# Optimization experiments

Hardware: AMD Instinct MI355X
Metric: run time of the kernel (lower is better)

## Reference

```python
import jax, jax.numpy as jnp
from jax import lax
import numpy as np

IN_DIM, HID, B, T = 64, 512, 256, 512


def _lstm_layer(xs, W_ih, W_hh, b_ih, b_hh):
    # xs: [B, T, D_in]; W_ih: [4H, D_in]; W_hh: [4H, H]; biases: [4H]
    Bn = xs.shape[0]
    H = W_hh.shape[1]
    # Precompute input projection for all timesteps (one big GEMM).
    x_proj = jnp.einsum('btd,gd->btg', xs, W_ih) + b_ih + b_hh  # [B, T, 4H]

    def step(carry, xp):
        h, c = carry
        g = xp + h @ W_hh.T  # [B, 4H], PyTorch gate order: i, f, g, o
        i, f, gg, o = jnp.split(g, 4, axis=-1)
        i = jax.nn.sigmoid(i)
        f = jax.nn.sigmoid(f)
        gg = jnp.tanh(gg)
        o = jax.nn.sigmoid(o)
        c = f * c + i * gg
        h = o * jnp.tanh(c)
        return (h, c), h

    z = jnp.zeros((Bn, H), xs.dtype)
    _, hs = lax.scan(step, (z, z), jnp.swapaxes(x_proj, 0, 1))  # [T, B, H]
    return jnp.swapaxes(hs, 0, 1)  # [B, T, H]


def setup_inputs() -> dict:
    key = jax.random.key(0)
    ks = jax.random.split(key, 16)
    s_in = 1.0 / np.sqrt(HID)
    u = lambda k, shp: jax.random.uniform(k, shp, jnp.float32, -s_in, s_in)
    return {
        'x': jax.random.normal(ks[0], (B, T, IN_DIM), jnp.float32),
        'W_ih0': u(ks[1], (4 * HID, IN_DIM)),
        'W_hh0': u(ks[2], (4 * HID, HID)),
        'b_ih0': u(ks[3], (4 * HID,)),
        'b_hh0': u(ks[4], (4 * HID,)),
        'W_ih1': u(ks[5], (4 * HID, HID)),
        'W_hh1': u(ks[6], (4 * HID, HID)),
        'b_ih1': u(ks[7], (4 * HID,)),
        'b_hh1': u(ks[8], (4 * HID,)),
        'W1': u(ks[9], (HID // 2, HID)),
        'b1': u(ks[10], (HID // 2,)),
        'W2': u(ks[11], (1, HID // 2)),
        'b2': u(ks[12], (1,)),
    }


def reference(x, W_ih0, W_hh0, b_ih0, b_hh0, W_ih1, W_hh1, b_ih1, b_hh1, W1, b1, W2, b2):
    h1 = _lstm_layer(x, W_ih0, W_hh0, b_ih0, b_hh0)   # [B, T, H]
    h2 = _lstm_layer(h1, W_ih1, W_hh1, b_ih1, b_hh1)  # [B, T, H] (inference: no inter-layer dropout)
    last = h2[:, -1, :]                                # final timestep
    hidden = jax.nn.relu(last @ W1.T + b1)
    return jax.nn.sigmoid(hidden @ W2.T + b2)          # [B, 1]
```

## Files before the change

### kernel.cpp

```cpp
#include <hip/hip_runtime.h>
#include <hip/hip_bf16.h>
#include <stdint.h>


#define Bsz 256
#define Tsz 512
#define IND 64
#define Hsz 512
#define BH (Bsz * Hsz)
#define P1S 66

typedef __attribute__((ext_vector_type(8))) short short8;
typedef __attribute__((ext_vector_type(4))) float floatx4;

static __device__ __forceinline__ short f2bf(float f) {
    unsigned u = __float_as_uint(f);
    u += 0x7FFFu + ((u >> 16) & 1u);
    return (short)(u >> 16);
}
static __device__ __forceinline__ float bf2f(short s) {
    return __uint_as_float(((unsigned)(unsigned short)s) << 16);
}
static __device__ __forceinline__ float sigm(float z) { return 1.f / (1.f + __expf(-z)); }
static __device__ __forceinline__ float tanh_f(float z) { return 2.f / (1.f + __expf(-2.f * z)) - 1.f; }

static __device__ __forceinline__ short8 ring16(const short* p) {
    short8 v;
    asm volatile("global_load_dwordx4 %0, %1, off sc1" : "=v"(v) : "v"(p));
    return v;
}

__global__ __launch_bounds__(512, 1) void lstm_pers(
    const float* __restrict__ x,
    const float* __restrict__ Wih0, const float* __restrict__ Whh0,
    const float* __restrict__ bih0, const float* __restrict__ bhh0,
    const float* __restrict__ Wih1, const float* __restrict__ Whh1,
    const float* __restrict__ bih1, const float* __restrict__ bhh1,
    int* __restrict__ slots, short* __restrict__ h1ring, short* __restrict__ h2ring)
{
    __shared__ __align__(16) char smem[131072 + 64 * P1S * 4];
    short* w  = (short*)smem;
    float* p1 = (float*)(smem + 131072);

    const int tid = threadIdx.x;
    const int bid = blockIdx.x;
    const int layer = bid >> 7;
    const int lb    = bid & 127;
    const int grp   = lb >> 5;
    const int chunk = lb & 31;
    const int sid   = layer * 32 + chunk;

    if (layer == 0) {
        for (int idx = tid; idx < 64 * 576; idx += 512) {
            int n = idx / 576, kc = idx - n * 576;
            int grow = (n >> 4) * Hsz + chunk * 16 + (n & 15);
            float v = (kc < IND) ? Wih0[grow * IND + kc]
                                 : Whh0[(size_t)grow * Hsz + kc - IND];
            w[n * 640 + (kc ^ ((n & 7) << 4))] = f2bf(v);
        }
    } else {
        for (int idx = tid; idx < 64 * 1024; idx += 512) {
            int n = idx >> 10, kc = idx & 1023;
            int grow = (n >> 4) * Hsz + chunk * 16 + (n & 15);
            float v = (kc < Hsz) ? Wih1[(size_t)grow * Hsz + kc]
                                 : Whh1[(size_t)grow * Hsz + kc - Hsz];
            w[n * 1024 + (kc ^ ((n & 7) << 4))] = f2bf(v);
        }
    }

    const int lane  = tid & 63;
    const int wv    = tid >> 6;
    const int mslot = wv >> 1;
    const int kh    = wv & 1;
    const int q     = lane >> 4;
    const int cl    = lane & 15;
    const int rowbase = grp * 64 + mslot * 16;
    const int hcol    = chunk * 16;

    float bI, bF, bG, bO;
    {
        const float* bi = layer ? bih1 : bih0;
        const float* bh = layer ? bhh1 : bhh0;
        int hix = hcol + cl;
        bI = bi[hix] + bh[hix];
        bF = bi[Hsz + hix] + bh[Hsz + hix];
        bG = bi[2 * Hsz + hix] + bh[2 * Hsz + hix];
        bO = bi[3 * Hsz + hix] + bh[3 * Hsz + hix];
    }

    __syncthreads();

    floatx4 c = {0.f, 0.f, 0.f, 0.f};
    const int* myslots = &slots[grp * 64 + lane];

    for (int k = 0; k <= Tsz; ++k) {
        const bool active = layer ? (k >= 1) : (k < Tsz);
        short8 af[16];

        if (active && layer == 0 && kh == 0) {
#pragma unroll
            for (int i = 0; i < 2; ++i) {
                const float* xp = x + ((size_t)(rowbase + cl) * Tsz + k) * IND + i * 32 + q * 8;
                floatx4 v0 = *(const floatx4*)xp;
                floatx4 v1 = *(const floatx4*)(xp + 4);
                short8 av;
                av[0] = f2bf(v0[0]); av[1] = f2bf(v0[1]); av[2] = f2bf(v0[2]); av[3] = f2bf(v0[3]);
                av[4] = f2bf(v1[0]); av[5] = f2bf(v1[1]); av[6] = f2bf(v1[2]); av[7] = f2bf(v1[3]);
                af[i] = av;
            }
        }

        if (k > 0) {
            int v = __hip_atomic_load(myslots, __ATOMIC_RELAXED, __HIP_MEMORY_SCOPE_AGENT);
            int spins = 0;
            while (v < k) {
                __builtin_amdgcn_s_sleep(1);
                v = __hip_atomic_load(myslots, __ATOMIC_RELAXED, __HIP_MEMORY_SCOPE_AGENT);
                if (++spins > (1 << 22)) break;
            }
            asm volatile("" ::: "memory");
        }

        floatx4 acc[4];
#pragma unroll
        for (int nt = 0; nt < 4; ++nt) acc[nt] = (floatx4){0.f, 0.f, 0.f, 0.f};

        if (active) {
            if (layer == 0) {
                const short* h1p = h1ring + (size_t)((k + 1) & 1) * BH;
                const short* abase = h1p + (size_t)(rowbase + cl) * Hsz + q * 8;
                if (kh == 0) {
#pragma unroll
                    for (int i = 2; i < 9; ++i) af[i] = ring16(abase + i * 32 - 64);
                } else {
#pragma unroll
                    for (int i = 0; i < 9; ++i) af[i] = ring16(abase + (9 + i) * 32 - 64);
                }
                asm volatile("s_waitcnt vmcnt(0)" ::: "memory");
                __builtin_amdgcn_sched_barrier(0);
#pragma unroll
                for (int i = 0; i < 9; ++i) {
                    const int kk = (kh * 9 + i) * 32;
#pragma unroll
                    for (int nt = 0; nt < 4; ++nt) {
                        const int n = nt * 16 + cl;
                        const int col = (kk + q * 8) ^ ((n & 7) << 4);
                        short8 bb = *(const short8*)&w[n * 640 + col];
                        acc[nt] = __builtin_amdgcn_mfma_f32_16x16x32_bf16(af[i], bb, acc[nt], 0, 0, 0);
                    }
                }
            } else {
                const short* h1p = h1ring + (size_t)((k + 1) & 1) * BH;
                const short* h2p = h2ring + (size_t)(k & 1) * BH;
                const short* src = (kh ? h2p : h1p) + (size_t)(rowbase + cl) * Hsz + q * 8;
#pragma unroll
                for (int i = 0; i < 16; ++i) af[i] = ring16(src + i * 32);
                asm volatile("s_waitcnt vmcnt(0)" ::: "memory");
                __builtin_amdgcn_sched_barrier(0);
#pragma unroll
                for (int i = 0; i < 16; ++i) {
                    const int kk = (kh * 16 + i) * 32;
#pragma unroll
                    for (int nt = 0; nt < 4; ++nt) {
                        const int n = nt * 16 + cl;
                        const int col = (kk + q * 8) ^ ((n & 7) << 4);
                        short8 bb = *(const short8*)&w[n * 1024 + col];
                        acc[nt] = __builtin_amdgcn_mfma_f32_16x16x32_bf16(af[i], bb, acc[nt], 0, 0, 0);
                    }
                }
            }
            if (kh) {
#pragma unroll
                for (int nt = 0; nt < 4; ++nt)
#pragma unroll
                    for (int r = 0; r < 4; ++r)
                        p1[(mslot * 16 + q * 4 + r) * P1S + nt * 16 + cl] = acc[nt][r];
            }
        }

        __syncthreads();

        if (active && kh == 0) {
            short* hout = layer ? (h2ring + (size_t)((k + 1) & 1) * BH)
                                : (h1ring + (size_t)(k & 1) * BH);
#pragma unroll
            for (int r = 0; r < 4; ++r) {
                const int prow = (mslot * 16 + q * 4 + r) * P1S;
                float iz = acc[0][r] + p1[prow + cl]      + bI;
                float fz = acc[1][r] + p1[prow + 16 + cl] + bF;
                float gz = acc[2][r] + p1[prow + 32 + cl] + bG;
                float oz = acc[3][r] + p1[prow + 48 + cl] + bO;
                float ii = sigm(iz);
                float ff = sigm(fz);
                float gg = tanh_f(gz);
                float oo = sigm(oz);
                float cn = ff * c[r] + ii * gg;
                c[r] = cn;
                float hv = oo * tanh_f(cn);
                __hip_atomic_store(&hout[(size_t)(rowbase + q * 4 + r) * Hsz + hcol + cl],
                                   f2bf(hv), __ATOMIC_RELAXED, __HIP_MEMORY_SCOPE_AGENT);
            }
        }

        __syncthreads();
        if (k < Tsz && tid == 0) {
            __hip_atomic_store(&slots[grp * 64 + sid], k + 1,
                               __ATOMIC_RELAXED, __HIP_MEMORY_SCOPE_AGENT);
        }
    }
}

__global__ void __launch_bounds__(256) head_kernel(
    const short* __restrict__ h2,
    const float* __restrict__ W1, const float* __restrict__ b1,
    const float* __restrict__ W2, const float* __restrict__ b2,
    float* __restrict__ out)
{
    __shared__ float hid[4][256];
    const int tid = threadIdx.x;
    const int r0 = blockIdx.x * 4;
    float acc[4] = {0.f, 0.f, 0.f, 0.f};
    const float* wrow = W1 + (size_t)tid * 512;
    for (int kk = 0; kk < 512; kk += 8) {
        float wv8[8];
#pragma unroll
        for (int j = 0; j < 8; ++j) wv8[j] = wrow[kk + j];
#pragma unroll
        for (int r = 0; r < 4; ++r) {
            short8 hv = *(const short8*)(h2 + (size_t)(r0 + r) * 512 + kk);
#pragma unroll
            for (int j = 0; j < 8; ++j) acc[r] += wv8[j] * bf2f(hv[j]);
        }
    }
#pragma unroll
    for (int r = 0; r < 4; ++r) hid[r][tid] = fmaxf(acc[r] + b1[tid], 0.f);
    __syncthreads();
    const int wv = tid >> 6, lane = tid & 63;
    float s = 0.f;
    for (int j = lane; j < 256; j += 64) s += hid[wv][j] * W2[j];
#pragma unroll
    for (int off = 32; off; off >>= 1) s += __shfl_down(s, off, 64);
    if (lane == 0) out[r0 + wv] = 1.f / (1.f + __expf(-(s + b2[0])));
}

extern "C" void kernel_launch(void* const* d_in, const int* in_sizes, int n_in,
                              void* d_out, int out_size, void* d_ws, size_t ws_size,
                              hipStream_t stream) {
    const float* x    = (const float*)d_in[0];
    const float* Wih0 = (const float*)d_in[1];
    const float* Whh0 = (const float*)d_in[2];
    const float* bih0 = (const float*)d_in[3];
    const float* bhh0 = (const float*)d_in[4];
    const float* Wih1 = (const float*)d_in[5];
    const float* Whh1 = (const float*)d_in[6];
    const float* bih1 = (const float*)d_in[7];
    const float* bhh1 = (const float*)d_in[8];
    const float* W1   = (const float*)d_in[9];
    const float* b1   = (const float*)d_in[10];
    const float* W2   = (const float*)d_in[11];
    const float* b2   = (const float*)d_in[12];
    float* out = (float*)d_out;

    const size_t SLOTS_BYTES = (size_t)4 * 64 * sizeof(int);
    const size_t RING_BYTES  = (size_t)2 * Bsz * Hsz * sizeof(short);
    if (ws_size < SLOTS_BYTES + 2 * RING_BYTES) return;

    char* ws = (char*)d_ws;
    int*   slots  = (int*)ws;
    short* h1ring = (short*)(ws + SLOTS_BYTES);
    short* h2ring = (short*)(ws + SLOTS_BYTES + RING_BYTES);

    hipMemsetAsync(d_ws, 0, SLOTS_BYTES + 2 * RING_BYTES, stream);

    void* args[] = {
        (void*)&x,
        (void*)&Wih0, (void*)&Whh0, (void*)&bih0, (void*)&bhh0,
        (void*)&Wih1, (void*)&Whh1, (void*)&bih1, (void*)&bhh1,
        (void*)&slots, (void*)&h1ring, (void*)&h2ring
    };
    hipLaunchCooperativeKernel((const void*)lstm_pers, dim3(256), dim3(512), args, 0, stream);

    const short* h2last = h2ring + (size_t)Bsz * Hsz;
    head_kernel<<<dim3(64), dim3(256), 0, stream>>>(h2last, W1, b1, W2, b2, out);
}
```

Baseline: 4.807 ms.

## Drop split-K waves and sync per-wave flags instead of block barriers

Cuts the block from 512 to 256 threads so each wave computes the full K reduction for its 16 rows. This removes the LDS partial-sum exchange and both __syncthreads per timestep. Synchronisation moves to per-wave slots: each wave publishes its own progress flag and waits on a ballot over the flags of the 64 producer blocks for its row group, so waves run ahead independently. The ring loads change from inline asm sc1 dwordx4 to pairs of relaxed atomic 64-bit loads. The cost is doubled serial MFMA work per wave, fewer waves to hide latency, and more flag traffic.

```diff
diff --git a/kernel.cpp b/kernel.cpp
--- a/kernel.cpp
+++ b/kernel.cpp
@@ -8,10 +8,10 @@
 #define IND 64
 #define Hsz 512
 #define BH (Bsz * Hsz)
-#define P1S 66
 
 typedef __attribute__((ext_vector_type(8))) short short8;
 typedef __attribute__((ext_vector_type(4))) float floatx4;
+typedef unsigned long long u64;
 
 static __device__ __forceinline__ short f2bf(float f) {
     unsigned u = __float_as_uint(f);
@@ -24,13 +24,14 @@
 static __device__ __forceinline__ float sigm(float z) { return 1.f / (1.f + __expf(-z)); }
 static __device__ __forceinline__ float tanh_f(float z) { return 2.f / (1.f + __expf(-2.f * z)) - 1.f; }
 
-static __device__ __forceinline__ short8 ring16(const short* p) {
-    short8 v;
-    asm volatile("global_load_dwordx4 %0, %1, off sc1" : "=v"(v) : "v"(p));
-    return v;
-}
-
-__global__ __launch_bounds__(512, 1) void lstm_pers(
+static __device__ __forceinline__ short8 ring_ld(const short* p) {
+    struct P { u64 a, b; } t;
+    t.a = __hip_atomic_load((const u64*)p,     __ATOMIC_RELAXED, __HIP_MEMORY_SCOPE_AGENT);
+    t.b = __hip_atomic_load((const u64*)p + 1, __ATOMIC_RELAXED, __HIP_MEMORY_SCOPE_AGENT);
+    return __builtin_bit_cast(short8, t);
+}
+
+__global__ __launch_bounds__(256, 1) void lstm_pers(
     const float* __restrict__ x,
     const float* __restrict__ Wih0, const float* __restrict__ Whh0,
     const float* __restrict__ bih0, const float* __restrict__ bhh0,
@@ -38,9 +39,7 @@
     const float* __restrict__ bih1, const float* __restrict__ bhh1,
     int* __restrict__ slots, short* __restrict__ h1ring, short* __restrict__ h2ring)
 {
-    __shared__ __align__(16) char smem[131072 + 64 * P1S * 4];
-    short* w  = (short*)smem;
-    float* p1 = (float*)(smem + 131072);
+    __shared__ __align__(16) short w[65536];
 
     const int tid = threadIdx.x;
     const int bid = blockIdx.x;
@@ -48,10 +47,9 @@
     const int lb    = bid & 127;
     const int grp   = lb >> 5;
     const int chunk = lb & 31;
-    const int sid   = layer * 32 + chunk;
 
     if (layer == 0) {
-        for (int idx = tid; idx < 64 * 576; idx += 512) {
+        for (int idx = tid; idx < 64 * 576; idx += 256) {
             int n = idx / 576, kc = idx - n * 576;
             int grow = (n >> 4) * Hsz + chunk * 16 + (n & 15);
             float v = (kc < IND) ? Wih0[grow * IND + kc]
@@ -59,7 +57,7 @@
             w[n * 640 + (kc ^ ((n & 7) << 4))] = f2bf(v);
         }
     } else {
-        for (int idx = tid; idx < 64 * 1024; idx += 512) {
+        for (int idx = tid; idx < 64 * 1024; idx += 256) {
             int n = idx >> 10, kc = idx & 1023;
             int grow = (n >> 4) * Hsz + chunk * 16 + (n & 15);
             float v = (kc < Hsz) ? Wih1[(size_t)grow * Hsz + kc]
@@ -70,11 +68,9 @@
 
     const int lane  = tid & 63;
     const int wv    = tid >> 6;
-    const int mslot = wv >> 1;
-    const int kh    = wv & 1;
     const int q     = lane >> 4;
     const int cl    = lane & 15;
-    const int rowbase = grp * 64 + mslot * 16;
+    const int rowbase = grp * 64 + wv * 16;
     const int hcol    = chunk * 16;
 
     float bI, bF, bG, bO;
@@ -91,105 +87,102 @@
     __syncthreads();
 
     floatx4 c = {0.f, 0.f, 0.f, 0.f};
-    const int* myslots = &slots[grp * 64 + lane];
+    const int sb = (grp * 4 + wv) * 64;
+    int* myslot = &slots[sb + layer * 32 + chunk];
+    const int* watch = &slots[sb + lane];
 
     for (int k = 0; k <= Tsz; ++k) {
         const bool active = layer ? (k >= 1) : (k < Tsz);
-        short8 af[16];
-
-        if (active && layer == 0 && kh == 0) {
-#pragma unroll
-            for (int i = 0; i < 2; ++i) {
-                const float* xp = x + ((size_t)(rowbase + cl) * Tsz + k) * IND + i * 32 + q * 8;
-                floatx4 v0 = *(const floatx4*)xp;
-                floatx4 v1 = *(const floatx4*)(xp + 4);
-                short8 av;
-                av[0] = f2bf(v0[0]); av[1] = f2bf(v0[1]); av[2] = f2bf(v0[2]); av[3] = f2bf(v0[3]);
-                av[4] = f2bf(v1[0]); av[5] = f2bf(v1[1]); av[6] = f2bf(v1[2]); av[7] = f2bf(v1[3]);
-                af[i] = av;
-            }
+
+        short8 ax0, ax1;
+        if (layer == 0 && active) {
+            const float* xp = x + ((size_t)(rowbase + cl) * Tsz + k) * IND + q * 8;
+            floatx4 v0 = *(const floatx4*)xp;
+            floatx4 v1 = *(const floatx4*)(xp + 4);
+            floatx4 v2 = *(const floatx4*)(xp + 32);
+            floatx4 v3 = *(const floatx4*)(xp + 36);
+            ax0[0] = f2bf(v0[0]); ax0[1] = f2bf(v0[1]); ax0[2] = f2bf(v0[2]); ax0[3] = f2bf(v0[3]);
+            ax0[4] = f2bf(v1[0]); ax0[5] = f2bf(v1[1]); ax0[6] = f2bf(v1[2]); ax0[7] = f2bf(v1[3]);
+            ax1[0] = f2bf(v2[0]); ax1[1] = f2bf(v2[1]); ax1[2] = f2bf(v2[2]); ax1[3] = f2bf(v2[3]);
+            ax1[4] = f2bf(v3[0]); ax1[5] = f2bf(v3[1]); ax1[6] = f2bf(v3[2]); ax1[7] = f2bf(v3[3]);
         }
 
         if (k > 0) {
-            int v = __hip_atomic_load(myslots, __ATOMIC_RELAXED, __HIP_MEMORY_SCOPE_AGENT);
+            int v = __hip_atomic_load(watch, __ATOMIC_RELAXED, __HIP_MEMORY_SCOPE_AGENT);
             int spins = 0;
-            while (v < k) {
+            while (__ballot(v < k)) {
                 __builtin_amdgcn_s_sleep(1);
-                v = __hip_atomic_load(myslots, __ATOMIC_RELAXED, __HIP_MEMORY_SCOPE_AGENT);
+                v = __hip_atomic_load(watch, __ATOMIC_RELAXED, __HIP_MEMORY_SCOPE_AGENT);
                 if (++spins > (1 << 22)) break;
             }
             asm volatile("" ::: "memory");
         }
 
-        floatx4 acc[4];
-#pragma unroll
-        for (int nt = 0; nt < 4; ++nt) acc[nt] = (floatx4){0.f, 0.f, 0.f, 0.f};
-
         if (active) {
+            floatx4 acc[4];
+#pragma unroll
+            for (int nt = 0; nt < 4; ++nt) acc[nt] = (floatx4){0.f, 0.f, 0.f, 0.f};
+
             if (layer == 0) {
                 const short* h1p = h1ring + (size_t)((k + 1) & 1) * BH;
-                const short* abase = h1p + (size_t)(rowbase + cl) * Hsz + q * 8;
-                if (kh == 0) {
-#pragma unroll
-                    for (int i = 2; i < 9; ++i) af[i] = ring16(abase + i * 32 - 64);
-                } else {
-#pragma unroll
-                    for (int i = 0; i < 9; ++i) af[i] = ring16(abase + (9 + i) * 32 - 64);
-                }
-                asm volatile("s_waitcnt vmcnt(0)" ::: "memory");
-                __builtin_amdgcn_sched_barrier(0);
-#pragma unroll
-                for (int i = 0; i < 9; ++i) {
-                    const int kk = (kh * 9 + i) * 32;
+                const short* ab  = h1p + (size_t)(rowbase + cl) * Hsz + q * 8;
+                short8 ah[16];
+#pragma unroll
+                for (int i = 0; i < 16; ++i) ah[i] = ring_ld(ab + i * 32);
+#pragma unroll
+                for (int ks = 0; ks < 18; ++ks) {
+                    const short8 a = (ks == 0) ? ax0 : (ks == 1) ? ax1 : ah[ks - 2];
+                    const int kk = ks * 32;
 #pragma unroll
                     for (int nt = 0; nt < 4; ++nt) {
                         const int n = nt * 16 + cl;
                         const int col = (kk + q * 8) ^ ((n & 7) << 4);
                         short8 bb = *(const short8*)&w[n * 640 + col];
-                        acc[nt] = __builtin_amdgcn_mfma_f32_16x16x32_bf16(af[i], bb, acc[nt], 0, 0, 0);
+                        acc[nt] = __builtin_amdgcn_mfma_f32_16x16x32_bf16(a, bb, acc[nt], 0, 0, 0);
                     }
                 }
             } else {
                 const short* h1p = h1ring + (size_t)((k + 1) & 1) * BH;
                 const short* h2p = h2ring + (size_t)(k & 1) * BH;
-                const short* src = (kh ? h2p : h1p) + (size_t)(rowbase + cl) * Hsz + q * 8;
-#pragma unroll
-                for (int i = 0; i < 16; ++i) af[i] = ring16(src + i * 32);
-                asm volatile("s_waitcnt vmcnt(0)" ::: "memory");
-                __builtin_amdgcn_sched_barrier(0);
-#pragma unroll
-                for (int i = 0; i < 16; ++i) {
-                    const int kk = (kh * 16 + i) * 32;
+                const short* b1a = h1p + (size_t)(rowbase + cl) * Hsz + q * 8;
+                const short* b2a = h2p + (size_t)(rowbase + cl) * Hsz + q * 8;
+                short8 a1[16], a2[16];
+#pragma unroll
+                for (int i = 0; i < 16; ++i) a1[i] = ring_ld(b1a + i * 32);
+#pragma unroll
+                for (int i = 0; i < 16; ++i) a2[i] = ring_ld(b2a + i * 32);
+#pragma unroll
+                for (int ks = 0; ks < 16; ++ks) {
+                    const int kk = ks * 32;
 #pragma unroll
                     for (int nt = 0; nt < 4; ++nt) {
                         const int n = nt * 16 + cl;
                         const int col = (kk + q * 8) ^ ((n & 7) << 4);
                         short8 bb = *(const short8*)&w[n * 1024 + col];
-                        acc[nt] = __builtin_amdgcn_mfma_f32_16x16x32_bf16(af[i], bb, acc[nt], 0, 0, 0);
+                        acc[nt] = __builtin_amdgcn_mfma_f32_16x16x32_bf16(a1[ks], bb, acc[nt], 0, 0, 0);
+                    }
+                }
+#pragma unroll
+                for (int ks = 16; ks < 32; ++ks) {
+                    const int kk = ks * 32;
+#pragma unroll
+                    for (int nt = 0; nt < 4; ++nt) {
+                        const int n = nt * 16 + cl;
+                        const int col = (kk + q * 8) ^ ((n & 7) << 4);
+                        short8 bb = *(const short8*)&w[n * 1024 + col];
+                        acc[nt] = __builtin_amdgcn_mfma_f32_16x16x32_bf16(a2[ks - 16], bb, acc[nt], 0, 0, 0);
                     }
                 }
             }
-            if (kh) {
-#pragma unroll
-                for (int nt = 0; nt < 4; ++nt)
-#pragma unroll
-                    for (int r = 0; r < 4; ++r)
-                        p1[(mslot * 16 + q * 4 + r) * P1S + nt * 16 + cl] = acc[nt][r];
-            }
-        }
-
-        __syncthreads();
-
-        if (active && kh == 0) {
+
             short* hout = layer ? (h2ring + (size_t)((k + 1) & 1) * BH)
                                 : (h1ring + (size_t)(k & 1) * BH);
 #pragma unroll
             for (int r = 0; r < 4; ++r) {
-                const int prow = (mslot * 16 + q * 4 + r) * P1S;
-                float iz = acc[0][r] + p1[prow + cl]      + bI;
-                float fz = acc[1][r] + p1[prow + 16 + cl] + bF;
-                float gz = acc[2][r] + p1[prow + 32 + cl] + bG;
-                float oz = acc[3][r] + p1[prow + 48 + cl] + bO;
+                float iz = acc[0][r] + bI;
+                float fz = acc[1][r] + bF;
+                float gz = acc[2][r] + bG;
+                float oz = acc[3][r] + bO;
                 float ii = sigm(iz);
                 float ff = sigm(fz);
                 float gg = tanh_f(gz);
@@ -202,10 +195,10 @@
             }
         }
 
-        __syncthreads();
-        if (k < Tsz && tid == 0) {
-            __hip_atomic_store(&slots[grp * 64 + sid], k + 1,
-                               __ATOMIC_RELAXED, __HIP_MEMORY_SCOPE_AGENT);
+        asm volatile("s_waitcnt vmcnt(0)" ::: "memory");
+        __builtin_amdgcn_sched_barrier(0);
+        if (lane == 0) {
+            __hip_atomic_store(myslot, k + 1, __ATOMIC_RELAXED, __HIP_MEMORY_SCOPE_AGENT);
         }
     }
 }
@@ -261,7 +254,7 @@
     const float* b2   = (const float*)d_in[12];
     float* out = (float*)d_out;
 
-    const size_t SLOTS_BYTES = (size_t)4 * 64 * sizeof(int);
+    const size_t SLOTS_BYTES = (size_t)1024 * sizeof(int);
     const size_t RING_BYTES  = (size_t)2 * Bsz * Hsz * sizeof(short);
     if (ws_size < SLOTS_BYTES + 2 * RING_BYTES) return;
 
@@ -278,7 +271,7 @@
         (void*)&Wih1, (void*)&Whh1, (void*)&bih1, (void*)&bhh1,
         (void*)&slots, (void*)&h1ring, (void*)&h2ring
     };
-    hipLaunchCooperativeKernel((const void*)lstm_pers, dim3(256), dim3(512), args, 0, stream);
+    hipLaunchCooperativeKernel((const void*)lstm_pers, dim3(256), dim3(256), args, 0, stream);
 
     const short* h2last = h2ring + (size_t)Bsz * Hsz;
     head_kernel<<<dim3(64), dim3(256), 0, stream>>>(h2last, W1, b1, W2, b2, out);
```

Measured after the change: 7.973 ms. +65.9%, slower.

## Poll dependency slots from one wave with ballot and acquire fence

Applied to the files above, without the earlier changes.

Only wave 0 of each block spins on the dependency slots, using a ballot across lanes, then issues an agent-scope acquire fence, and the block is released through __syncthreads. The inline-asm sc1 ring loads and their explicit vmcnt wait and sched_barrier are replaced by ordinary vector loads, which the compiler can schedule and overlap with the MFMAs. This cuts polling traffic from every wave and relies on the acquire fence for visibility. It adds one block barrier per step and depends on the fence invalidating stale cache lines, which is a correctness risk if it does not.

```diff
diff --git a/kernel.cpp b/kernel.cpp
--- a/kernel.cpp
+++ b/kernel.cpp
@@ -23,12 +23,6 @@
 }
 static __device__ __forceinline__ float sigm(float z) { return 1.f / (1.f + __expf(-z)); }
 static __device__ __forceinline__ float tanh_f(float z) { return 2.f / (1.f + __expf(-2.f * z)) - 1.f; }
-
-static __device__ __forceinline__ short8 ring16(const short* p) {
-    short8 v;
-    asm volatile("global_load_dwordx4 %0, %1, off sc1" : "=v"(v) : "v"(p));
-    return v;
-}
 
 __global__ __launch_bounds__(512, 1) void lstm_pers(
     const float* __restrict__ x,
@@ -91,7 +85,7 @@
     __syncthreads();
 
     floatx4 c = {0.f, 0.f, 0.f, 0.f};
-    const int* myslots = &slots[grp * 64 + lane];
+    const int* watch = &slots[grp * 64 + lane];
 
     for (int k = 0; k <= Tsz; ++k) {
         const bool active = layer ? (k >= 1) : (k < Tsz);
@@ -110,16 +104,19 @@
             }
         }
 
-        if (k > 0) {
-            int v = __hip_atomic_load(myslots, __ATOMIC_RELAXED, __HIP_MEMORY_SCOPE_AGENT);
-            int spins = 0;
-            while (v < k) {
-                __builtin_amdgcn_s_sleep(1);
-                v = __hip_atomic_load(myslots, __ATOMIC_RELAXED, __HIP_MEMORY_SCOPE_AGENT);
-                if (++spins > (1 << 22)) break;
-            }
-            asm volatile("" ::: "memory");
-        }
+        if (wv == 0) {
+            if (k > 0) {
+                int v = __hip_atomic_load(watch, __ATOMIC_RELAXED, __HIP_MEMORY_SCOPE_AGENT);
+                int spins = 0;
+                while (__ballot(v < k)) {
+                    __builtin_amdgcn_s_sleep(1);
+                    v = __hip_atomic_load(watch, __ATOMIC_RELAXED, __HIP_MEMORY_SCOPE_AGENT);
+                    if (++spins > (1 << 22)) break;
+                }
+            }
+            __builtin_amdgcn_fence(__ATOMIC_ACQUIRE, "agent");
+        }
+        __syncthreads();
 
         floatx4 acc[4];
 #pragma unroll
@@ -128,16 +125,14 @@
         if (active) {
             if (layer == 0) {
                 const short* h1p = h1ring + (size_t)((k + 1) & 1) * BH;
-                const short* abase = h1p + (size_t)(rowbase + cl) * Hsz + q * 8;
+                const short* ab  = h1p + (size_t)(rowbase + cl) * Hsz + q * 8;
                 if (kh == 0) {
 #pragma unroll
-                    for (int i = 2; i < 9; ++i) af[i] = ring16(abase + i * 32 - 64);
+                    for (int i = 2; i < 9; ++i) af[i] = *(const short8*)(ab + i * 32 - 64);
                 } else {
 #pragma unroll
-                    for (int i = 0; i < 9; ++i) af[i] = ring16(abase + (9 + i) * 32 - 64);
-                }
-                asm volatile("s_waitcnt vmcnt(0)" ::: "memory");
-                __builtin_amdgcn_sched_barrier(0);
+                    for (int i = 0; i < 9; ++i) af[i] = *(const short8*)(ab + (9 + i) * 32 - 64);
+                }
 #pragma unroll
                 for (int i = 0; i < 9; ++i) {
                     const int kk = (kh * 9 + i) * 32;
@@ -154,9 +149,7 @@
                 const short* h2p = h2ring + (size_t)(k & 1) * BH;
                 const short* src = (kh ? h2p : h1p) + (size_t)(rowbase + cl) * Hsz + q * 8;
 #pragma unroll
-                for (int i = 0; i < 16; ++i) af[i] = ring16(src + i * 32);
-                asm volatile("s_waitcnt vmcnt(0)" ::: "memory");
-                __builtin_amdgcn_sched_barrier(0);
+                for (int i = 0; i < 16; ++i) af[i] = *(const short8*)(src + i * 32);
 #pragma unroll
                 for (int i = 0; i < 16; ++i) {
                     const int kk = (kh * 16 + i) * 32;
@@ -216,6 +209,7 @@
     const float* __restrict__ W2, const float* __restrict__ b2,
     float* __restrict__ out)
 {
+    __builtin_amdgcn_fence(__ATOMIC_ACQUIRE, "agent");
     __shared__ float hid[4][256];
     const int tid = threadIdx.x;
     const int r0 = blockIdx.x * 4;
@@ -261,7 +255,7 @@
     const float* b2   = (const float*)d_in[12];
     float* out = (float*)d_out;
 
-    const size_t SLOTS_BYTES = (size_t)4 * 64 * sizeof(int);
+    const size_t SLOTS_BYTES = (size_t)1024 * sizeof(int);
     const size_t RING_BYTES  = (size_t)2 * Bsz * Hsz * sizeof(short);
     if (ws_size < SLOTS_BYTES + 2 * RING_BYTES) return;
 
```

New measurement: 4.609 ms. 1.04x faster.
